# Optimization experiments

Hardware: AMD Instinct MI355X
Metric: run time of the kernel (lower is better)

## Reference

```python
import jax, jax.numpy as jnp
import numpy as np

DIM = 2048
N_HEADS = 16
HEAD_DIM = DIM // N_HEADS  # 128
MAX_LEN = 2048
B, T = 2, 2048
RESTORE_SCALE = DIM ** 0.5  # sqkinit / sqkscale = 1 / (1/sqrt(dim))
SQK_SCALE = 1.0 / DIM ** 0.5


def _rope_tables(seq_len, head_dim, dtype=jnp.float32):
    d2 = head_dim // 2
    pos = jnp.arange(seq_len, dtype=dtype)                     # [T]
    theta = 1.0 / (10000.0 ** (jnp.arange(0, head_dim, 2, dtype=dtype) / head_dim))  # [d2]
    ang = pos[:, None] * theta[None, :]                        # [T, d2]
    return jnp.cos(ang), jnp.sin(ang)


def _apply_rope(x, cos, sin):
    # x: [B, H, T, D]; cos/sin: [T, D/2] broadcast over B,H
    d2 = x.shape[-1] // 2
    xr, xi = x[..., :d2], x[..., d2:]
    return jnp.concatenate([xr * cos - xi * sin, xr * sin + xi * cos], axis=-1)


def setup_inputs() -> dict:
    key = jax.random.key(0)
    ks = jax.random.split(key, 5)
    s = 0.02
    return {
        "x":  jax.random.normal(ks[0], (B, T, DIM), jnp.float32),
        "Wq": jax.random.normal(ks[1], (DIM, DIM), jnp.float32) * s,
        "Wk": jax.random.normal(ks[2], (DIM, DIM), jnp.float32) * s,
        "Wv": jax.random.normal(ks[3], (DIM, DIM), jnp.float32) * s,
        "Wo": jax.random.normal(ks[4], (DIM, DIM), jnp.float32) * s,
        "sqk": jnp.ones((N_HEADS, 1, HEAD_DIM), jnp.float32) * SQK_SCALE,
    }


def reference(x, Wq, Wk, Wv, Wo, sqk):
    Bc, Tc, C = x.shape
    # QKV projections (torch Linear: x @ W.T), split heads -> [B, H, T, D]
    def proj(W):
        return (x @ W.T).reshape(Bc, Tc, N_HEADS, HEAD_DIM).transpose(0, 2, 1, 3)
    q, k, v = proj(Wq), proj(Wk), proj(Wv)

    cos, sin = _rope_tables(Tc, HEAD_DIM, x.dtype)
    actual_sqk = sqk * RESTORE_SCALE  # [H, 1, D]
    q = _apply_rope(q, cos, sin) * actual_sqk
    k = _apply_rope(k, cos, sin) * actual_sqk

    # SDPA with scale = sqrt(head_dim) (as in the source, not 1/sqrt)
    scale = HEAD_DIM ** 0.5
    scores = jnp.einsum("bhtd,bhsd->bhts", q, k) * scale  # [B, H, T, T]
    causal = jnp.tril(jnp.ones((Tc, Tc), bool))
    scores = jnp.where(causal, scores, -jnp.inf)
    attn = jax.nn.softmax(scores, axis=-1)
    out = jnp.einsum("bhts,bhsd->bhtd", attn, v)           # [B, H, T, D]
    out = out.transpose(0, 2, 1, 3).reshape(Bc, Tc, C)

    y = out @ Wo.T
    # F.normalize(p=2, dim=-1, eps=1e-12)
    norm = jnp.linalg.norm(y, axis=-1, keepdims=True)
    return y / jnp.maximum(norm, 1e-12)
```

## Files before the change

### kernel.cpp

```cpp
#include <hip/hip_runtime.h>

#define DEVFN __device__ __forceinline__

typedef float    floatx4 __attribute__((ext_vector_type(4)));
typedef _Float16 half8   __attribute__((ext_vector_type(8)));
typedef _Float16 half4v  __attribute__((ext_vector_type(4)));

#define MFMA16H(a, b, c) __builtin_amdgcn_mfma_f32_16x16x32_f16((a), (b), (c), 0, 0, 0)

DEVFN void async16(void* lds, const void* g) {
  __builtin_amdgcn_global_load_lds(
      (const __attribute__((address_space(1))) unsigned int*)g,
      (__attribute__((address_space(3))) unsigned int*)lds, 16, 0, 0);
}
DEVFN half8 ld8h(const _Float16* p) { return *(const half8*)p; }

__global__ __launch_bounds__(256) void cvt_prep(
    const float4* __restrict__ x, const float4* __restrict__ wq,
    const float4* __restrict__ wk, const float4* __restrict__ wv,
    const float4* __restrict__ wo,
    half4v* __restrict__ xh, half4v* __restrict__ xl,
    half4v* __restrict__ qo, half4v* __restrict__ ko,
    half4v* __restrict__ vo, half4v* __restrict__ oo,
    float* __restrict__ cosT, float* __restrict__ sinT) {
  int i = blockIdx.x * 256 + threadIdx.x;
  {
    float4 v = x[i];
    half4v h = {(_Float16)v.x, (_Float16)v.y, (_Float16)v.z, (_Float16)v.w};
    half4v l = {(_Float16)(v.x - (float)h.x), (_Float16)(v.y - (float)h.y),
                (_Float16)(v.z - (float)h.z), (_Float16)(v.w - (float)h.w)};
    xh[i] = h;
    xl[i] = l;
  }
  if (i < 1048576) {
    float4 v = wq[i];
    qo[i] = (half4v){(_Float16)v.x, (_Float16)v.y, (_Float16)v.z, (_Float16)v.w};
    v = wk[i];
    ko[i] = (half4v){(_Float16)v.x, (_Float16)v.y, (_Float16)v.z, (_Float16)v.w};
    v = wv[i];
    vo[i] = (half4v){(_Float16)v.x, (_Float16)v.y, (_Float16)v.z, (_Float16)v.w};
    v = wo[i];
    oo[i] = (half4v){(_Float16)v.x, (_Float16)v.y, (_Float16)v.z, (_Float16)v.w};
  }
  if (i < 131072) {
    int t = i >> 6, d = i & 63;
    double theta = exp(-((double)(2 * d) / 128.0) * log(10000.0));
    double ang = (double)t * theta;
    cosT[i] = (float)cos(ang);
    sinT[i] = (float)sin(ang);
  }
}

__global__ __launch_bounds__(512, 2) void gemm_qk_f16(
    const _Float16* __restrict__ xhp, const _Float16* __restrict__ xlp,
    const _Float16* __restrict__ wqp, const _Float16* __restrict__ wkp,
    const float* __restrict__ cosT, const float* __restrict__ sinT,
    const float* __restrict__ sqk,
    _Float16* __restrict__ qhi, _Float16* __restrict__ qlo,
    _Float16* __restrict__ khi) {
  constexpr int Kd = 2048, NT = 64;
  const int n0 = blockIdx.x * 128, m0 = blockIdx.y * 256;
  const int tid = threadIdx.x, w = tid >> 6, lane = tid & 63;
  const int quad = lane >> 4, l16 = lane & 15;
  const int c0 = w & 1, rb = w >> 1, rgb = rb * 4;
  const int cgr0 = 2 * c0, cgr1 = 2 * c0 + 1, cgr2 = 2 * c0 + 4, cgr3 = 2 * c0 + 5;

  __shared__ __align__(16) _Float16 smem[57344];
  _Float16* XH = smem;
  _Float16* XL = smem + 16384;
  _Float16* WQ = smem + 32768;
  _Float16* WK = smem + 45056;

  floatx4 accQ[4][4], accK[4][4];
#pragma unroll
  for (int i = 0; i < 4; i++)
#pragma unroll
    for (int c = 0; c < 4; c++) {
      accQ[i][c] = (floatx4){0.f, 0.f, 0.f, 0.f};
      accK[i][c] = (floatx4){0.f, 0.f, 0.f, 0.f};
    }

  const size_t xg0 = (size_t)(m0 + 32 * w + l16) * Kd + quad * 8;
  const size_t xg1 = xg0 + (size_t)16 * Kd;
  const size_t wg = (size_t)(n0 + 16 * w + l16) * Kd + quad * 8;

#define STAGE_X(T)                                                      \
  {                                                                     \
    const int kk_ = (T) * 32;                                           \
    _Float16* bx_ = XH + ((T) & 1) * 8192;                              \
    _Float16* bl_ = XL + ((T) & 1) * 8192;                              \
    async16(bx_ + (2 * w) * 512, xhp + xg0 + kk_);                      \
    async16(bx_ + (2 * w + 1) * 512, xhp + xg1 + kk_);                  \
    async16(bl_ + (2 * w) * 512, xlp + xg0 + kk_);                      \
    async16(bl_ + (2 * w + 1) * 512, xlp + xg1 + kk_);                  \
  }
#define STAGE_W(T)                                                      \
  {                                                                     \
    const int kk_ = (T) * 32;                                           \
    async16(WQ + ((T) % 3) * 4096 + w * 512, wqp + wg + kk_);           \
    async16(WK + ((T) % 3) * 4096 + w * 512, wkp + wg + kk_);           \
  }

  STAGE_X(0);
  STAGE_W(0);
  STAGE_W(1);
  asm volatile("s_waitcnt vmcnt(2)" ::: "memory");
  __builtin_amdgcn_s_barrier();

#pragma unroll 1
  for (int t = 0; t < NT; ++t) {
    const _Float16* XH_ = XH + (t & 1) * 8192;
    const _Float16* XL_ = XL + (t & 1) * 8192;
    const _Float16* WQ_ = WQ + (t % 3) * 4096;
    const _Float16* WK_ = WK + (t % 3) * 4096;

    half8 ah[4], al[4], bq[4];
#pragma unroll
    for (int i = 0; i < 4; i++) {
      ah[i] = ld8h(XH_ + (rgb + i) * 512 + lane * 8);
      al[i] = ld8h(XL_ + (rgb + i) * 512 + lane * 8);
    }
    bq[0] = ld8h(WQ_ + cgr0 * 512 + lane * 8);
    bq[1] = ld8h(WQ_ + cgr1 * 512 + lane * 8);
    bq[2] = ld8h(WQ_ + cgr2 * 512 + lane * 8);
    bq[3] = ld8h(WQ_ + cgr3 * 512 + lane * 8);
    if (t + 1 < NT) STAGE_X(t + 1);
    __builtin_amdgcn_s_barrier();
    asm volatile("s_waitcnt lgkmcnt(0)");
    __builtin_amdgcn_sched_barrier(0);
    __builtin_amdgcn_s_setprio(1);
#pragma unroll
    for (int i = 0; i < 4; i++)
#pragma unroll
      for (int c = 0; c < 4; c++)
        accQ[i][c] = MFMA16H(ah[i], bq[c], accQ[i][c]);
#pragma unroll
    for (int i = 0; i < 4; i++)
#pragma unroll
      for (int c = 0; c < 4; c++)
        accQ[i][c] = MFMA16H(al[i], bq[c], accQ[i][c]);
    __builtin_amdgcn_s_setprio(0);
    __builtin_amdgcn_s_barrier();

    half8 bk[4];
    bk[0] = ld8h(WK_ + cgr0 * 512 + lane * 8);
    bk[1] = ld8h(WK_ + cgr1 * 512 + lane * 8);
    bk[2] = ld8h(WK_ + cgr2 * 512 + lane * 8);
    bk[3] = ld8h(WK_ + cgr3 * 512 + lane * 8);
    if (t + 2 < NT) STAGE_W(t + 2);
    __builtin_amdgcn_s_barrier();
    asm volatile("s_waitcnt lgkmcnt(0)");
    __builtin_amdgcn_sched_barrier(0);
    __builtin_amdgcn_s_setprio(1);
#pragma unroll
    for (int i = 0; i < 4; i++)
#pragma unroll
      for (int c = 0; c < 4; c++)
        accK[i][c] = MFMA16H(ah[i], bk[c], accK[i][c]);
#pragma unroll
    for (int i = 0; i < 4; i++)
#pragma unroll
      for (int c = 0; c < 4; c++)
        accK[i][c] = MFMA16H(al[i], bk[c], accK[i][c]);
    __builtin_amdgcn_s_setprio(0);

    if (t + 2 < NT) {
      asm volatile("s_waitcnt vmcnt(2)" ::: "memory");
    } else {
      asm volatile("s_waitcnt vmcnt(0)" ::: "memory");
    }
    __builtin_amdgcn_s_barrier();
  }
#undef STAGE_X
#undef STAGE_W

  _Float16* stH = smem + w * 1152;
  _Float16* stL = smem + 9216 + w * 1152;

  const int h = n0 >> 7;
  const int b = m0 >> 11;

#pragma unroll
  for (int rg = 0; rg < 4; rg++) {
    const int tt0 = (m0 & 2047) + rb * 64 + rg * 16;
    const size_t gbase = (((size_t)(b * 16 + h)) * 2048 + tt0) * 128;

#pragma unroll
    for (int cj = 0; cj < 2; cj++) {
      int d = c0 * 32 + cj * 16 + l16;
      float s1 = sqk[h * 128 + d] * 512.0f;
      float s2 = sqk[h * 128 + d + 64] * 512.0f;
#pragma unroll
      for (int r = 0; r < 4; r++) {
        int tq = tt0 + quad * 4 + r;
        float cc = cosT[tq * 64 + d], sn = sinT[tq * 64 + d];
        float xr = accQ[rg][cj][r], xi = accQ[rg][cj + 2][r];
        float o1 = (xr * cc - xi * sn) * s1;
        float o2 = (xr * sn + xi * cc) * s2;
        _Float16 h1 = (_Float16)o1, h2 = (_Float16)o2;
        int rl = quad * 4 + r;
        stH[rl * 72 + cj * 16 + l16] = h1;
        stH[rl * 72 + 32 + cj * 16 + l16] = h2;
        stL[rl * 72 + cj * 16 + l16] = (_Float16)(o1 - (float)h1);
        stL[rl * 72 + 32 + cj * 16 + l16] = (_Float16)(o2 - (float)h2);
      }
    }
#pragma unroll
    for (int it = 0; it < 2; it++) {
      int row = it * 8 + (lane >> 3), pc = (lane & 7) * 8;
      int d = (pc < 32) ? (c0 * 32 + pc) : (64 + c0 * 32 + (pc - 32));
      size_t ga = gbase + (size_t)row * 128 + d;
      *(half8*)(qhi + ga) = ld8h(&stH[row * 72 + pc]);
      *(half8*)(qlo + ga) = ld8h(&stL[row * 72 + pc]);
    }

#pragma unroll
    for (int cj = 0; cj < 2; cj++) {
      int d = c0 * 32 + cj * 16 + l16;
      float s1 = sqk[h * 128 + d] * 45.254834f;
      float s2 = sqk[h * 128 + d + 64] * 45.254834f;
#pragma unroll
      for (int r = 0; r < 4; r++) {
        int tq = tt0 + quad * 4 + r;
        float cc = cosT[tq * 64 + d], sn = sinT[tq * 64 + d];
        float xr = accK[rg][cj][r], xi = accK[rg][cj + 2][r];
        int rl = quad * 4 + r;
        stH[rl * 72 + cj * 16 + l16] = (_Float16)((xr * cc - xi * sn) * s1);
        stH[rl * 72 + 32 + cj * 16 + l16] = (_Float16)((xr * sn + xi * cc) * s2);
      }
    }
#pragma unroll
    for (int it = 0; it < 2; it++) {
      int row = it * 8 + (lane >> 3), pc = (lane & 7) * 8;
      int d = (pc < 32) ? (c0 * 32 + pc) : (64 + c0 * 32 + (pc - 32));
      *(half8*)(khi + gbase + (size_t)row * 128 + d) = ld8h(&stH[row * 72 + pc]);
    }
  }
}

__global__ __launch_bounds__(512, 2) void gemm_v_f16(
    const _Float16* __restrict__ xhp, const _Float16* __restrict__ wvp,
    _Float16* __restrict__ vt) {
  constexpr int Kd = 2048, NT = 64;
  const int n0 = blockIdx.x * 128, m0 = blockIdx.y * 256;
  const int tid = threadIdx.x, w = tid >> 6, lane = tid & 63;
  const int quad = lane >> 4, l16 = lane & 15;
  const int c0 = w & 1, rb = w >> 1, rgb = rb * 4;

  __shared__ __align__(16) _Float16 smem[28672];
  _Float16* XH = smem;
  _Float16* WV = smem + 16384;

  floatx4 accV[4][4];
#pragma unroll
  for (int i = 0; i < 4; i++)
#pragma unroll
    for (int c = 0; c < 4; c++) accV[i][c] = (floatx4){0.f, 0.f, 0.f, 0.f};

  const size_t xg0 = (size_t)(m0 + 32 * w + l16) * Kd + quad * 8;
  const size_t xg1 = xg0 + (size_t)16 * Kd;
  const size_t wg = (size_t)(n0 + 16 * w + l16) * Kd + quad * 8;

#define STAGE_XV(T)                                                     \
  {                                                                     \
    const int kk_ = (T) * 32;                                           \
    _Float16* bx_ = XH + ((T) & 1) * 8192;                              \
    async16(bx_ + (2 * w) * 512, xhp + xg0 + kk_);                      \
    async16(bx_ + (2 * w + 1) * 512, xhp + xg1 + kk_);                  \
  }
#define STAGE_WV(T)                                                     \
  { async16(WV + ((T) % 3) * 4096 + w * 512, wvp + wg + (T) * 32); }

  STAGE_XV(0);
  STAGE_WV(0);
  STAGE_WV(1);
  asm volatile("s_waitcnt vmcnt(1)" ::: "memory");
  __builtin_amdgcn_s_barrier();

#pragma unroll 1
  for (int t = 0; t < NT; ++t) {
    const _Float16* XH_ = XH + (t & 1) * 8192;
    const _Float16* WV_ = WV + (t % 3) * 4096;

    half8 ah[4], bv[4];
#pragma unroll
    for (int i = 0; i < 4; i++)
      ah[i] = ld8h(XH_ + (rgb + i) * 512 + lane * 8);
#pragma unroll
    for (int c = 0; c < 4; c++)
      bv[c] = ld8h(WV_ + (4 * c0 + c) * 512 + lane * 8);
    if (t + 1 < NT) STAGE_XV(t + 1);
    if (t + 2 < NT) STAGE_WV(t + 2);
    __builtin_amdgcn_s_barrier();
    asm volatile("s_waitcnt lgkmcnt(0)");
    __builtin_amdgcn_sched_barrier(0);
    __builtin_amdgcn_s_setprio(1);
#pragma unroll
    for (int i = 0; i < 4; i++)
#pragma unroll
      for (int c = 0; c < 4; c++)
        accV[i][c] = MFMA16H(ah[i], bv[c], accV[i][c]);
    __builtin_amdgcn_s_setprio(0);
    if (t + 2 < NT) {
      asm volatile("s_waitcnt vmcnt(1)" ::: "memory");
    } else {
      asm volatile("s_waitcnt vmcnt(0)" ::: "memory");
    }
    __builtin_amdgcn_s_barrier();
  }
#undef STAGE_XV
#undef STAGE_WV

  _Float16* stV = smem + w * 1024;

  const int h = n0 >> 7;
  const int b = m0 >> 11;
  const int bh = b * 16 + h;

#pragma unroll
  for (int rg = 0; rg < 4; rg++) {
    const int tt0 = (m0 & 2047) + rb * 64 + rg * 16;
#pragma unroll
    for (int c = 0; c < 4; c++)
#pragma unroll
      for (int r = 0; r < 4; r++)
        stV[(c * 16 + l16) * 16 + quad * 4 + r] = (_Float16)accV[rg][c][r];
#pragma unroll
    for (int it = 0; it < 2; it++) {
      int dl = it * 32 + (lane >> 1), th = (lane & 1) * 8;
      int dh = c0 * 64 + dl;
      size_t ga = ((size_t)bh * 128 + dh) * 2048 + tt0 + th;
      *(half8*)(vt + ga) = ld8h(&stV[dl * 16 + th]);
    }
  }
}

__global__ __launch_bounds__(256, 2) void flash_attn(
    const _Float16* __restrict__ qhp, const _Float16* __restrict__ qlp,
    const _Float16* __restrict__ khp,
    const _Float16* __restrict__ vtp, _Float16* __restrict__ aout) {
  constexpr int T = 2048, HD = 128;
  const int bh = blockIdx.x;
  const int qt = 31 - blockIdx.y;
  const int q0 = qt * 64;
  const int tid = threadIdx.x, w = tid >> 6, lane = tid & 63;
  const int quad = lane >> 4, l16 = lane & 15;

  __shared__ __align__(16) _Float16 Kh[2][8192];
  __shared__ __align__(16) _Float16 Vt[2][8192];
  __shared__ __align__(16) _Float16 Pb[4][16 * 72];

  const size_t qkbase = (size_t)bh * T * HD;
  const size_t vbase = (size_t)bh * HD * T;

  auto stageKV = [&](int kt, int set) {
    const int s0 = kt * 64;
    for (int c = w; c < 16; c += 4) {
      int tt = c >> 2, ss = c & 3;
      size_t go = qkbase + (size_t)(s0 + tt * 16 + l16) * HD + ss * 32 + quad * 8;
      async16(&Kh[set][c * 512], khp + go);
      int dt = c >> 1, vs = c & 1;
      size_t vo = vbase + (size_t)(dt * 16 + l16) * T + s0 + vs * 32 + quad * 8;
      async16(&Vt[set][c * 512], vtp + vo);
    }
  };

  half8 qh[4], ql[4];
#pragma unroll
  for (int s = 0; s < 4; s++) {
    size_t off = qkbase + (size_t)(q0 + w * 16 + l16) * HD + s * 32 + quad * 8;
    qh[s] = *(const half8*)(qhp + off);
    ql[s] = *(const half8*)(qlp + off);
  }

  floatx4 o[8];
#pragma unroll
  for (int dt = 0; dt < 8; dt++) o[dt] = (floatx4){0.f, 0.f, 0.f, 0.f};
  float mrow[4], lrow[4];
#pragma unroll
  for (int r = 0; r < 4; r++) { mrow[r] = -3e38f; lrow[r] = 0.f; }

  const int ntiles = qt + 1;

  stageKV(0, 0);
  __syncthreads();

#pragma unroll 1
  for (int kt = 0; kt < ntiles; ++kt) {
    const int s0 = kt * 64;
    const int set = kt & 1;
    if (kt + 1 < ntiles) stageKV(kt + 1, set ^ 1);

    floatx4 S[4];
#pragma unroll
    for (int j = 0; j < 4; j++) S[j] = (floatx4){0.f, 0.f, 0.f, 0.f};

    __builtin_amdgcn_s_setprio(1);
#pragma unroll
    for (int s = 0; s < 4; s++) {
#pragma unroll
      for (int j = 0; j < 4; j++) {
        half8 kh = ld8h(&Kh[set][(j * 4 + s) * 512 + lane * 8]);
        S[j] = MFMA16H(qh[s], kh, S[j]);
        S[j] = MFMA16H(ql[s], kh, S[j]);
      }
    }
    __builtin_amdgcn_s_setprio(0);

    if (kt == ntiles - 1) {
      int rbase = q0 + w * 16 + quad * 4;
#pragma unroll
      for (int j = 0; j < 4; j++) {
        int cg = s0 + j * 16 + l16;
#pragma unroll
        for (int r = 0; r < 4; r++)
          if (cg > rbase + r) S[j][r] = -3e38f;
      }
    }

    float lm[4];
#pragma unroll
    for (int r = 0; r < 4; r++)
      lm[r] = fmaxf(fmaxf(S[0][r], S[1][r]), fmaxf(S[2][r], S[3][r]));

    bool ok = true;
#pragma unroll
    for (int r = 0; r < 4; r++) ok = ok && (lm[r] <= mrow[r] + 8.0f);

    if (!__all(ok ? 1 : 0)) {
#pragma unroll
      for (int d = 1; d < 16; d <<= 1)
#pragma unroll
        for (int r = 0; r < 4; r++)
          lm[r] = fmaxf(lm[r], __shfl_xor(lm[r], d, 64));
#pragma unroll
      for (int r = 0; r < 4; r++) {
        float mnew = fmaxf(mrow[r], lm[r]);
        float al = __expf(mrow[r] - mnew);
        mrow[r] = mnew;
        lrow[r] *= al;
#pragma unroll
        for (int dt = 0; dt < 8; dt++) o[dt][r] *= al;
      }
    }

    float rs[4];
#pragma unroll
    for (int r = 0; r < 4; r++) {
      float e0 = __expf(S[0][r] - mrow[r]);
      float e1 = __expf(S[1][r] - mrow[r]);
      float e2 = __expf(S[2][r] - mrow[r]);
      float e3 = __expf(S[3][r] - mrow[r]);
      S[0][r] = e0; S[1][r] = e1; S[2][r] = e2; S[3][r] = e3;
      rs[r] = (e0 + e1) + (e2 + e3);
    }
#pragma unroll
    for (int d = 1; d < 16; d <<= 1)
#pragma unroll
      for (int r = 0; r < 4; r++) rs[r] += __shfl_xor(rs[r], d, 64);
#pragma unroll
    for (int r = 0; r < 4; r++) lrow[r] += rs[r];

    half8 pf[2];
#pragma unroll
    for (int r = 0; r < 4; r++)
#pragma unroll
      for (int j = 0; j < 4; j++)
        Pb[w][(quad * 4 + r) * 72 + j * 16 + l16] = (_Float16)S[j][r];
    pf[0] = ld8h(&Pb[w][l16 * 72 + quad * 8]);
    pf[1] = ld8h(&Pb[w][l16 * 72 + 32 + quad * 8]);

    __builtin_amdgcn_s_setprio(1);
#pragma unroll
    for (int dt = 0; dt < 8; dt++) {
#pragma unroll
      for (int s = 0; s < 2; s++) {
        half8 vf = ld8h(&Vt[set][(dt * 2 + s) * 512 + lane * 8]);
        o[dt] = MFMA16H(pf[s], vf, o[dt]);
      }
    }
    __builtin_amdgcn_s_setprio(0);
    __syncthreads();
  }

  const int b = bh >> 4, h = bh & 15;
#pragma unroll
  for (int r = 0; r < 4; r++) {
    int trow = q0 + w * 16 + quad * 4 + r;
    float linv = 1.0f / lrow[r];
    size_t base = ((size_t)(b * T + trow)) * 2048 + h * 128;
#pragma unroll
    for (int dt = 0; dt < 8; dt++)
      aout[base + dt * 16 + l16] = (_Float16)(o[dt][r] * linv);
  }
}

__global__ __launch_bounds__(256, 2) void gemm_o_f16(
    const _Float16* __restrict__ A, const _Float16* __restrict__ B,
    float* __restrict__ outF) {
  constexpr int Kd = 2048;
  constexpr int Nd = 2048;
  const int n0 = blockIdx.x * 128, m0 = blockIdx.y * 128;
  const int tid = threadIdx.x, w = tid >> 6, lane = tid & 63;
  const int quad = lane >> 4, l16 = lane & 15;

  __shared__ __align__(16) _Float16 As[8192];
  __shared__ __align__(16) _Float16 Bs[8192];

  floatx4 acc[2][8];
#pragma unroll
  for (int i = 0; i < 2; i++)
#pragma unroll
    for (int j = 0; j < 8; j++) acc[i][j] = (floatx4){0.f, 0.f, 0.f, 0.f};

  const int t0 = 2 * w, t1 = 2 * w + 1;
  const size_t ao0 = (size_t)(m0 + t0 * 16 + l16) * Kd + quad * 8;
  const size_t ao1 = (size_t)(m0 + t1 * 16 + l16) * Kd + quad * 8;
  const size_t bo0 = (size_t)(n0 + t0 * 16 + l16) * Kd + quad * 8;
  const size_t bo1 = (size_t)(n0 + t1 * 16 + l16) * Kd + quad * 8;

  for (int k0 = 0; k0 < Kd; k0 += 64) {
    __syncthreads();
    async16(&As[t0 * 512], A + ao0 + k0);
    async16(&As[t1 * 512], A + ao1 + k0);
    async16(&As[4096 + t0 * 512], A + ao0 + k0 + 32);
    async16(&As[4096 + t1 * 512], A + ao1 + k0 + 32);
    async16(&Bs[t0 * 512], B + bo0 + k0);
    async16(&Bs[t1 * 512], B + bo1 + k0);
    async16(&Bs[4096 + t0 * 512], B + bo0 + k0 + 32);
    async16(&Bs[4096 + t1 * 512], B + bo1 + k0 + 32);
    __syncthreads();
    half8 a00 = ld8h(&As[t0 * 512 + lane * 8]);
    half8 a10 = ld8h(&As[t1 * 512 + lane * 8]);
    half8 a01 = ld8h(&As[4096 + t0 * 512 + lane * 8]);
    half8 a11 = ld8h(&As[4096 + t1 * 512 + lane * 8]);
#pragma unroll
    for (int j = 0; j < 8; j++) {
      half8 b0 = ld8h(&Bs[j * 512 + lane * 8]);
      acc[0][j] = MFMA16H(a00, b0, acc[0][j]);
      acc[1][j] = MFMA16H(a10, b0, acc[1][j]);
      half8 b1 = ld8h(&Bs[4096 + j * 512 + lane * 8]);
      acc[0][j] = MFMA16H(a01, b1, acc[0][j]);
      acc[1][j] = MFMA16H(a11, b1, acc[1][j]);
    }
  }

#pragma unroll
  for (int i = 0; i < 2; i++) {
    int rbase = m0 + (2 * w + i) * 16 + quad * 4;
#pragma unroll
    for (int j = 0; j < 8; j++) {
      int col = n0 + j * 16 + l16;
#pragma unroll
      for (int r = 0; r < 4; r++)
        outF[(size_t)(rbase + r) * Nd + col] = acc[i][j][r];
    }
  }
}

__global__ __launch_bounds__(256) void rownorm(const float* __restrict__ y,
                                               float* __restrict__ out) {
  int row = blockIdx.x;
  const float4* yr = (const float4*)(y + (size_t)row * 2048);
  float4* od = (float4*)(out + (size_t)row * 2048);
  int t = threadIdx.x;
  float4 v0 = yr[t], v1 = yr[t + 256];
  float ss = v0.x * v0.x + v0.y * v0.y + v0.z * v0.z + v0.w * v0.w +
             v1.x * v1.x + v1.y * v1.y + v1.z * v1.z + v1.w * v1.w;
#pragma unroll
  for (int d = 1; d < 64; d <<= 1) ss += __shfl_xor(ss, d, 64);
  __shared__ float red[4];
  if ((t & 63) == 0) red[t >> 6] = ss;
  __syncthreads();
  float tot = red[0] + red[1] + red[2] + red[3];
  float inv = 1.0f / fmaxf(sqrtf(tot), 1e-12f);
  v0.x *= inv; v0.y *= inv; v0.z *= inv; v0.w *= inv;
  v1.x *= inv; v1.y *= inv; v1.z *= inv; v1.w *= inv;
  od[t] = v0;
  od[t + 256] = v1;
}

extern "C" void kernel_launch(void* const* d_in, const int* in_sizes, int n_in,
                              void* d_out, int out_size, void* d_ws, size_t ws_size,
                              hipStream_t stream) {
  (void)in_sizes; (void)n_in; (void)out_size; (void)ws_size;
  const float* x   = (const float*)d_in[0];
  const float* Wq  = (const float*)d_in[1];
  const float* Wk  = (const float*)d_in[2];
  const float* Wv  = (const float*)d_in[3];
  const float* Wo  = (const float*)d_in[4];
  const float* sqk = (const float*)d_in[5];
  char* ws = (char*)d_ws;

  constexpr size_t SZX = 8388608ull * 2;
  constexpr size_t SZW = 4194304ull * 2;

  size_t o_xh = 0;
  size_t o_xl = o_xh + SZX;
  size_t o_wq = o_xl + SZX;
  size_t o_wk = o_wq + SZW;
  size_t o_wv = o_wk + SZW;
  size_t o_wo = o_wv + SZW;
  size_t o_qh = o_wo + SZW;
  size_t o_ql = o_qh + SZX;
  size_t o_kh = o_ql + SZX;
  size_t o_v  = o_kh + SZX;
  size_t o_vt = o_v + SZX;
  size_t o_cos = o_vt + SZX;
  size_t o_sin = o_cos + 2048 * 64 * 4;
  size_t o_aout = o_wq;
  size_t o_y    = o_qh;

  _Float16* xh = (_Float16*)(ws + o_xh);
  _Float16* xl = (_Float16*)(ws + o_xl);
  _Float16* wq = (_Float16*)(ws + o_wq);
  _Float16* wk = (_Float16*)(ws + o_wk);
  _Float16* wv = (_Float16*)(ws + o_wv);
  _Float16* wo = (_Float16*)(ws + o_wo);
  _Float16* qh = (_Float16*)(ws + o_qh);
  _Float16* ql = (_Float16*)(ws + o_ql);
  _Float16* kh = (_Float16*)(ws + o_kh);
  _Float16* vt = (_Float16*)(ws + o_vt);
  float* cosT = (float*)(ws + o_cos);
  float* sinT = (float*)(ws + o_sin);
  _Float16* aout = (_Float16*)(ws + o_aout);
  float* y = (float*)(ws + o_y);

  cvt_prep<<<8192, 256, 0, stream>>>((const float4*)x, (const float4*)Wq,
                                     (const float4*)Wk, (const float4*)Wv,
                                     (const float4*)Wo, (half4v*)xh, (half4v*)xl,
                                     (half4v*)wq, (half4v*)wk, (half4v*)wv,
                                     (half4v*)wo, cosT, sinT);

  gemm_qk_f16<<<dim3(16, 16), 512, 0, stream>>>(xh, xl, wq, wk, cosT, sinT,
                                                sqk, qh, ql, kh);
  gemm_v_f16<<<dim3(16, 16), 512, 0, stream>>>(xh, wv, vt);

  flash_attn<<<dim3(32, 32), 256, 0, stream>>>(qh, ql, kh, vt, aout);

  gemm_o_f16<<<dim3(16, 32), 256, 0, stream>>>(aout, wo, y);
  rownorm<<<4096, 256, 0, stream>>>(y, (float*)d_out);
}
```

Before: 496.5 us.

## Drop mid-iteration barriers in QK/V GEMMs and pipeline output projection GEMM

The QK and V projection loops drop their mid-iteration barriers and lgkmcnt waits, issuing all LDS reads and next-stage async loads up front and running the Q and K MFMAs back to back. A sched_barrier is added after each loop barrier, plus a __syncthreads before the epilogue reuses shared memory. The output projection GEMM is rewritten from a synchronous 128x128 tile with 256 threads into a 256x128 tile with 512 threads, double-buffered A and triple-buffered W staging. This aims to cut barrier stalls and overlap global loads with MFMA work. Relying on implicit LDS read ordering without an explicit lgkmcnt wait before the MFMAs is a correctness risk.

```diff
diff --git a/kernel.cpp b/kernel.cpp
--- a/kernel.cpp
+++ b/kernel.cpp
@@ -106,6 +106,7 @@
   STAGE_W(1);
   asm volatile("s_waitcnt vmcnt(2)" ::: "memory");
   __builtin_amdgcn_s_barrier();
+  __builtin_amdgcn_sched_barrier(0);
 
 #pragma unroll 1
   for (int t = 0; t < NT; ++t) {
@@ -114,7 +115,7 @@
     const _Float16* WQ_ = WQ + (t % 3) * 4096;
     const _Float16* WK_ = WK + (t % 3) * 4096;
 
-    half8 ah[4], al[4], bq[4];
+    half8 ah[4], al[4], bq[4], bk[4];
 #pragma unroll
     for (int i = 0; i < 4; i++) {
       ah[i] = ld8h(XH_ + (rgb + i) * 512 + lane * 8);
@@ -124,34 +125,23 @@
     bq[1] = ld8h(WQ_ + cgr1 * 512 + lane * 8);
     bq[2] = ld8h(WQ_ + cgr2 * 512 + lane * 8);
     bq[3] = ld8h(WQ_ + cgr3 * 512 + lane * 8);
-    if (t + 1 < NT) STAGE_X(t + 1);
-    __builtin_amdgcn_s_barrier();
-    asm volatile("s_waitcnt lgkmcnt(0)");
-    __builtin_amdgcn_sched_barrier(0);
-    __builtin_amdgcn_s_setprio(1);
-#pragma unroll
-    for (int i = 0; i < 4; i++)
-#pragma unroll
-      for (int c = 0; c < 4; c++)
-        accQ[i][c] = MFMA16H(ah[i], bq[c], accQ[i][c]);
-#pragma unroll
-    for (int i = 0; i < 4; i++)
-#pragma unroll
-      for (int c = 0; c < 4; c++)
-        accQ[i][c] = MFMA16H(al[i], bq[c], accQ[i][c]);
-    __builtin_amdgcn_s_setprio(0);
-    __builtin_amdgcn_s_barrier();
-
-    half8 bk[4];
     bk[0] = ld8h(WK_ + cgr0 * 512 + lane * 8);
     bk[1] = ld8h(WK_ + cgr1 * 512 + lane * 8);
     bk[2] = ld8h(WK_ + cgr2 * 512 + lane * 8);
     bk[3] = ld8h(WK_ + cgr3 * 512 + lane * 8);
+    if (t + 1 < NT) STAGE_X(t + 1);
     if (t + 2 < NT) STAGE_W(t + 2);
-    __builtin_amdgcn_s_barrier();
-    asm volatile("s_waitcnt lgkmcnt(0)");
-    __builtin_amdgcn_sched_barrier(0);
     __builtin_amdgcn_s_setprio(1);
+#pragma unroll
+    for (int i = 0; i < 4; i++)
+#pragma unroll
+      for (int c = 0; c < 4; c++)
+        accQ[i][c] = MFMA16H(ah[i], bq[c], accQ[i][c]);
+#pragma unroll
+    for (int i = 0; i < 4; i++)
+#pragma unroll
+      for (int c = 0; c < 4; c++)
+        accQ[i][c] = MFMA16H(al[i], bq[c], accQ[i][c]);
 #pragma unroll
     for (int i = 0; i < 4; i++)
 #pragma unroll
@@ -170,10 +160,12 @@
       asm volatile("s_waitcnt vmcnt(0)" ::: "memory");
     }
     __builtin_amdgcn_s_barrier();
+    __builtin_amdgcn_sched_barrier(0);
   }
 #undef STAGE_X
 #undef STAGE_W
 
+  __syncthreads();
   _Float16* stH = smem + w * 1152;
   _Float16* stL = smem + 9216 + w * 1152;
 
@@ -276,6 +268,7 @@
   STAGE_WV(1);
   asm volatile("s_waitcnt vmcnt(1)" ::: "memory");
   __builtin_amdgcn_s_barrier();
+  __builtin_amdgcn_sched_barrier(0);
 
 #pragma unroll 1
   for (int t = 0; t < NT; ++t) {
@@ -291,9 +284,6 @@
       bv[c] = ld8h(WV_ + (4 * c0 + c) * 512 + lane * 8);
     if (t + 1 < NT) STAGE_XV(t + 1);
     if (t + 2 < NT) STAGE_WV(t + 2);
-    __builtin_amdgcn_s_barrier();
-    asm volatile("s_waitcnt lgkmcnt(0)");
-    __builtin_amdgcn_sched_barrier(0);
     __builtin_amdgcn_s_setprio(1);
 #pragma unroll
     for (int i = 0; i < 4; i++)
@@ -307,10 +297,12 @@
       asm volatile("s_waitcnt vmcnt(0)" ::: "memory");
     }
     __builtin_amdgcn_s_barrier();
+    __builtin_amdgcn_sched_barrier(0);
   }
 #undef STAGE_XV
 #undef STAGE_WV
 
+  __syncthreads();
   _Float16* stV = smem + w * 1024;
 
   const int h = n0 >> 7;
@@ -495,65 +487,87 @@
   }
 }
 
-__global__ __launch_bounds__(256, 2) void gemm_o_f16(
-    const _Float16* __restrict__ A, const _Float16* __restrict__ B,
+__global__ __launch_bounds__(512, 2) void gemm_o_f16(
+    const _Float16* __restrict__ A, const _Float16* __restrict__ Bw,
     float* __restrict__ outF) {
-  constexpr int Kd = 2048;
-  constexpr int Nd = 2048;
-  const int n0 = blockIdx.x * 128, m0 = blockIdx.y * 128;
+  constexpr int Kd = 2048, NT = 64;
+  const int n0 = blockIdx.x * 128, m0 = blockIdx.y * 256;
   const int tid = threadIdx.x, w = tid >> 6, lane = tid & 63;
   const int quad = lane >> 4, l16 = lane & 15;
-
-  __shared__ __align__(16) _Float16 As[8192];
-  __shared__ __align__(16) _Float16 Bs[8192];
-
-  floatx4 acc[2][8];
-#pragma unroll
-  for (int i = 0; i < 2; i++)
-#pragma unroll
-    for (int j = 0; j < 8; j++) acc[i][j] = (floatx4){0.f, 0.f, 0.f, 0.f};
-
-  const int t0 = 2 * w, t1 = 2 * w + 1;
-  const size_t ao0 = (size_t)(m0 + t0 * 16 + l16) * Kd + quad * 8;
-  const size_t ao1 = (size_t)(m0 + t1 * 16 + l16) * Kd + quad * 8;
-  const size_t bo0 = (size_t)(n0 + t0 * 16 + l16) * Kd + quad * 8;
-  const size_t bo1 = (size_t)(n0 + t1 * 16 + l16) * Kd + quad * 8;
-
-  for (int k0 = 0; k0 < Kd; k0 += 64) {
-    __syncthreads();
-    async16(&As[t0 * 512], A + ao0 + k0);
-    async16(&As[t1 * 512], A + ao1 + k0);
-    async16(&As[4096 + t0 * 512], A + ao0 + k0 + 32);
-    async16(&As[4096 + t1 * 512], A + ao1 + k0 + 32);
-    async16(&Bs[t0 * 512], B + bo0 + k0);
-    async16(&Bs[t1 * 512], B + bo1 + k0);
-    async16(&Bs[4096 + t0 * 512], B + bo0 + k0 + 32);
-    async16(&Bs[4096 + t1 * 512], B + bo1 + k0 + 32);
-    __syncthreads();
-    half8 a00 = ld8h(&As[t0 * 512 + lane * 8]);
-    half8 a10 = ld8h(&As[t1 * 512 + lane * 8]);
-    half8 a01 = ld8h(&As[4096 + t0 * 512 + lane * 8]);
-    half8 a11 = ld8h(&As[4096 + t1 * 512 + lane * 8]);
-#pragma unroll
-    for (int j = 0; j < 8; j++) {
-      half8 b0 = ld8h(&Bs[j * 512 + lane * 8]);
-      acc[0][j] = MFMA16H(a00, b0, acc[0][j]);
-      acc[1][j] = MFMA16H(a10, b0, acc[1][j]);
-      half8 b1 = ld8h(&Bs[4096 + j * 512 + lane * 8]);
-      acc[0][j] = MFMA16H(a01, b1, acc[0][j]);
-      acc[1][j] = MFMA16H(a11, b1, acc[1][j]);
-    }
-  }
-
-#pragma unroll
-  for (int i = 0; i < 2; i++) {
-    int rbase = m0 + (2 * w + i) * 16 + quad * 4;
-#pragma unroll
-    for (int j = 0; j < 8; j++) {
-      int col = n0 + j * 16 + l16;
+  const int c0 = w & 1, rb = w >> 1, rgb = rb * 4;
+
+  __shared__ __align__(16) _Float16 smem[28672];
+  _Float16* AH = smem;
+  _Float16* WB = smem + 16384;
+
+  floatx4 acc[4][4];
+#pragma unroll
+  for (int i = 0; i < 4; i++)
+#pragma unroll
+    for (int c = 0; c < 4; c++) acc[i][c] = (floatx4){0.f, 0.f, 0.f, 0.f};
+
+  const size_t ag0 = (size_t)(m0 + 32 * w + l16) * Kd + quad * 8;
+  const size_t ag1 = ag0 + (size_t)16 * Kd;
+  const size_t wg = (size_t)(n0 + 16 * w + l16) * Kd + quad * 8;
+
+#define STAGE_A(T)                                                      \
+  {                                                                     \
+    const int kk_ = (T) * 32;                                           \
+    _Float16* b_ = AH + ((T) & 1) * 8192;                               \
+    async16(b_ + (2 * w) * 512, A + ag0 + kk_);                         \
+    async16(b_ + (2 * w + 1) * 512, A + ag1 + kk_);                     \
+  }
+#define STAGE_B(T)                                                      \
+  { async16(WB + ((T) % 3) * 4096 + w * 512, Bw + wg + (T) * 32); }
+
+  STAGE_A(0);
+  STAGE_B(0);
+  STAGE_B(1);
+  asm volatile("s_waitcnt vmcnt(1)" ::: "memory");
+  __builtin_amdgcn_s_barrier();
+  __builtin_amdgcn_sched_barrier(0);
+
+#pragma unroll 1
+  for (int t = 0; t < NT; ++t) {
+    const _Float16* AH_ = AH + (t & 1) * 8192;
+    const _Float16* WB_ = WB + (t % 3) * 4096;
+
+    half8 a[4], b[4];
+#pragma unroll
+    for (int i = 0; i < 4; i++)
+      a[i] = ld8h(AH_ + (rgb + i) * 512 + lane * 8);
+#pragma unroll
+    for (int c = 0; c < 4; c++)
+      b[c] = ld8h(WB_ + (4 * c0 + c) * 512 + lane * 8);
+    if (t + 1 < NT) STAGE_A(t + 1);
+    if (t + 2 < NT) STAGE_B(t + 2);
+    __builtin_amdgcn_s_setprio(1);
+#pragma unroll
+    for (int i = 0; i < 4; i++)
+#pragma unroll
+      for (int c = 0; c < 4; c++)
+        acc[i][c] = MFMA16H(a[i], b[c], acc[i][c]);
+    __builtin_amdgcn_s_setprio(0);
+    if (t + 2 < NT) {
+      asm volatile("s_waitcnt vmcnt(1)" ::: "memory");
+    } else {
+      asm volatile("s_waitcnt vmcnt(0)" ::: "memory");
+    }
+    __builtin_amdgcn_s_barrier();
+    __builtin_amdgcn_sched_barrier(0);
+  }
+#undef STAGE_A
+#undef STAGE_B
+
+#pragma unroll
+  for (int i = 0; i < 4; i++) {
+    int rbase = m0 + (rgb + i) * 16 + quad * 4;
+#pragma unroll
+    for (int c = 0; c < 4; c++) {
+      int col = n0 + (4 * c0 + c) * 16 + l16;
 #pragma unroll
       for (int r = 0; r < 4; r++)
-        outF[(size_t)(rbase + r) * Nd + col] = acc[i][j][r];
+        outF[(size_t)(rbase + r) * 2048 + col] = acc[i][c][r];
     }
   }
 }
@@ -638,6 +652,6 @@
 
   flash_attn<<<dim3(32, 32), 256, 0, stream>>>(qh, ql, kh, vt, aout);
 
-  gemm_o_f16<<<dim3(16, 32), 256, 0, stream>>>(aout, wo, y);
+  gemm_o_f16<<<dim3(16, 16), 512, 0, stream>>>(aout, wo, y);
   rownorm<<<4096, 256, 0, stream>>>(y, (float*)d_out);
 }
```

After: 500.8 us. About the same (+0.9%).
